# Kernel tuning notes

Measured on AMD Instinct MI355X. Metric: run time of the kernel, lower is better.

The kernel has to match this reference:

```python
import jax, jax.numpy as jnp
import numpy as np
from jax.scipy.special import logsumexp

B, S, V, T = 32, 128, 8, 66  # batch, seq_len, predicates per example, num_tags


def setup_inputs() -> dict:
    key = jax.random.key(0)
    k0, k1, k2, k3, k4, k5 = jax.random.split(key, 6)
    score = jax.random.normal(k0, (B, S, S, T), dtype=jnp.float32)
    v_label = jax.random.randint(k1, (B, V), 0, S)
    role_label = jax.random.randint(k2, (B, V, S), 0, T)
    transitions = jax.random.normal(k3, (T, T), dtype=jnp.float32) * 0.1
    start_transitions = jax.random.normal(k4, (T,), dtype=jnp.float32) * 0.1
    end_transitions = jax.random.normal(k5, (T,), dtype=jnp.float32) * 0.1
    return {
        "score": score,
        "transitions": transitions,
        "start_transitions": start_transitions,
        "end_transitions": end_transitions,
        "v_label": v_label,
        "role_label": role_label,
    }


def reference(score, transitions, start_transitions, end_transitions, v_label, role_label):
    b, s, _, t = score.shape
    v = v_label.shape[1]
    # gather predicate rows: a_score[i] = score[i].index_select(0, v_label[i])  -> [B*V, S, T]
    emissions = jnp.take_along_axis(score, v_label[:, :, None, None], axis=1).reshape(b * v, s, t)
    tags = role_label.reshape(b * v, s)

    # --- gold (numerator) score ---
    emit_sc = jnp.take_along_axis(emissions, tags[..., None], axis=-1).squeeze(-1).sum(-1)  # [BV]
    trans_sc = transitions[tags[:, :-1], tags[:, 1:]].sum(-1)  # [BV]
    gold = start_transitions[tags[:, 0]] + emit_sc + trans_sc + end_transitions[tags[:, -1]]

    # --- log partition via forward algorithm (fused logsumexp scan) ---
    alpha0 = start_transitions[None, :] + emissions[:, 0]  # [BV, T]

    def step(alpha, emit_t):
        # alpha[:, i] + transitions[i, j] -> logsumexp over i, add emission at t
        alpha = logsumexp(alpha[:, :, None] + transitions[None, :, :], axis=1) + emit_t
        return alpha, None

    alphaT, _ = jax.lax.scan(step, alpha0, jnp.swapaxes(emissions[:, 1:], 0, 1))
    log_z = logsumexp(alphaT + end_transitions[None, :], axis=-1)  # [BV]

    nll = jnp.sum(log_z - gold)
    normalizer = jnp.asarray(b * v, dtype=nll.dtype)  # num_prop with gold predicates
    return nll / normalizer
```

## Files before the change

### kernel.cpp

```cpp
#include <hip/hip_runtime.h>
#include <hip/hip_bf16.h>

constexpr int TT = 66;
constexpr int SS = 128;
constexpr int NV = 8;

__device__ __forceinline__ float rl(float v, int lane) {
    return __int_as_float(__builtin_amdgcn_readlane(__float_as_int(v), lane));
}

__global__ __launch_bounds__(128) void crf_chain_kernel(
    const float* __restrict__ score,
    const float* __restrict__ trans,
    const float* __restrict__ startt,
    const float* __restrict__ endt,
    const int*   __restrict__ v_label,
    const int*   __restrict__ role_label,
    float*       __restrict__ ws_nll)
{
    __shared__ __align__(16) float xl[SS * TT];
    __shared__ float gbuf[TT + 2];
    const int tid  = threadIdx.x;
    const int lane = tid & 63;
    const int wid  = tid >> 6;
    const int bv   = blockIdx.x;
    const int b    = bv >> 3;
    const int v    = bv & 7;

    const int prow = v_label[b * NV + v];
    const float* src = score + ((size_t)(b * SS + prow) * (SS * TT));
    const float4* src4 = reinterpret_cast<const float4*>(src);
    float4* dst4 = reinterpret_cast<float4*>(xl);
    const int base4 = wid * 1056;
    #pragma unroll
    for (int k = 0; k < 16; ++k) {
        const int idx = base4 + k * 64 + lane;
        float4 tv = src4[idx];
        tv.x = __expf(tv.x); tv.y = __expf(tv.y);
        tv.z = __expf(tv.z); tv.w = __expf(tv.w);
        dst4[idx] = tv;
    }
    if (lane < 32) {
        const int idx = base4 + 1024 + lane;
        float4 tv = src4[idx];
        tv.x = __expf(tv.x); tv.y = __expf(tv.y);
        tv.z = __expf(tv.z); tv.w = __expf(tv.w);
        dst4[idx] = tv;
    }

    const int* tags = role_label + bv * SS;
    float gold = 0.f;
    if (wid == 0) {
        const int s0 = lane;
        const int tg0 = tags[s0];
        gold += src[s0 * TT + tg0];
        gold += trans[tg0 * TT + tags[s0 + 1]];
        const int s1 = lane + 64;
        const int tg1 = tags[s1];
        gold += src[s1 * TT + tg1];
        if (lane < 63) gold += trans[tg1 * TT + tags[s1 + 1]];
        #pragma unroll
        for (int off = 32; off; off >>= 1) gold += __shfl_xor(gold, off);
        gold += startt[tags[0]] + endt[tags[SS - 1]];
    }

    const int xsel = (lane == 1) ? 65 : 64;
    float W[TT], W2[TT];
    if (wid == 0) {
        #pragma unroll
        for (int i = 0; i < TT; ++i) {
            W[i]  = __expf(trans[i * TT + lane]);
            W2[i] = __expf(trans[i * TT + xsel]);
        }
    } else {
        #pragma unroll
        for (int j = 0; j < TT; ++j) {
            W[j]  = __expf(trans[lane * TT + j]);
            W2[j] = __expf(trans[xsel * TT + j]);
        }
    }

    int esum = 0;
    float F = 0.f, F64 = 0.f, F65 = 0.f;
    if (wid == 0) {
        F   = __expf(startt[lane]) * xl[lane];
        F64 = __expf(startt[64])   * xl[64];
        F65 = __expf(startt[65])   * xl[65];
        float xc   = xl[TT + lane];
        float xc64 = xl[TT + 64];
        float xc65 = xl[TT + 65];
        #pragma unroll 1
        for (int t = 1; t <= 63; ++t) {
            const int tn = (t < 63) ? t + 1 : t;
            const float xn   = xl[tn * TT + lane];
            const float xn64 = xl[tn * TT + 64];
            const float xn65 = xl[tn * TT + 65];

            float acc0 = F64 * W[64],  acc1 = F65 * W[65];
            float acc2 = 0.f,          acc3 = 0.f;
            float ex0  = F64 * W2[64], ex1  = F65 * W2[65];
            float ex2  = 0.f,          ex3  = 0.f;
            #pragma unroll
            for (int i = 0; i < 64; i += 4) {
                const float a0 = rl(F, i + 0);
                const float a1 = rl(F, i + 1);
                const float a2 = rl(F, i + 2);
                const float a3 = rl(F, i + 3);
                acc0 = fmaf(a0, W[i + 0], acc0);  ex0 = fmaf(a0, W2[i + 0], ex0);
                acc1 = fmaf(a1, W[i + 1], acc1);  ex1 = fmaf(a1, W2[i + 1], ex1);
                acc2 = fmaf(a2, W[i + 2], acc2);  ex2 = fmaf(a2, W2[i + 2], ex2);
                acc3 = fmaf(a3, W[i + 3], acc3);  ex3 = fmaf(a3, W2[i + 3], ex3);
            }
            const float S  = (acc0 + acc1) + (acc2 + acc3);
            const float Sx = (ex0 + ex1) + (ex2 + ex3);
            const float S64 = rl(Sx, 0);
            const float S65 = rl(Sx, 1);

            const int sbits = __builtin_amdgcn_readfirstlane(__float_as_int(S));
            const int e = ((sbits >> 23) & 0xff) - 127;
            esum += e;
            const float r = __int_as_float((127 - e) << 23);

            F   = (S   * r) * xc;
            F64 = (S64 * r) * xc64;
            F65 = (S65 * r) * xc65;
            xc = xn; xc64 = xn64; xc65 = xn65;
        }
    } else {
        float G   = __expf(endt[lane]);
        float G64 = __expf(endt[64]);
        float G65 = __expf(endt[65]);
        float xc   = xl[127 * TT + lane];
        float xc64 = xl[127 * TT + 64];
        float xc65 = xl[127 * TT + 65];
        #pragma unroll 1
        for (int t = 127; t >= 64; --t) {
            const int tn = (t > 64) ? t - 1 : t;
            const float xn   = xl[tn * TT + lane];
            const float xn64 = xl[tn * TT + 64];
            const float xn65 = xl[tn * TT + 65];

            const float Y   = G * xc;
            const float Y64 = G64 * xc64;
            const float Y65 = G65 * xc65;

            float acc0 = Y64 * W[64],  acc1 = Y65 * W[65];
            float acc2 = 0.f,          acc3 = 0.f;
            float ex0  = Y64 * W2[64], ex1  = Y65 * W2[65];
            float ex2  = 0.f,          ex3  = 0.f;
            #pragma unroll
            for (int j = 0; j < 64; j += 4) {
                const float y0 = rl(Y, j + 0);
                const float y1 = rl(Y, j + 1);
                const float y2 = rl(Y, j + 2);
                const float y3 = rl(Y, j + 3);
                acc0 = fmaf(y0, W[j + 0], acc0);  ex0 = fmaf(y0, W2[j + 0], ex0);
                acc1 = fmaf(y1, W[j + 1], acc1);  ex1 = fmaf(y1, W2[j + 1], ex1);
                acc2 = fmaf(y2, W[j + 2], acc2);  ex2 = fmaf(y2, W2[j + 2], ex2);
                acc3 = fmaf(y3, W[j + 3], acc3);  ex3 = fmaf(y3, W2[j + 3], ex3);
            }
            const float S  = (acc0 + acc1) + (acc2 + acc3);
            const float Sx = (ex0 + ex1) + (ex2 + ex3);
            const float S64 = rl(Sx, 0);
            const float S65 = rl(Sx, 1);

            const int sbits = __builtin_amdgcn_readfirstlane(__float_as_int(S));
            const int e = ((sbits >> 23) & 0xff) - 127;
            esum += e;
            const float r = __int_as_float((127 - e) << 23);

            G   = S   * r;
            G64 = S64 * r;
            G65 = S65 * r;
            xc = xn; xc64 = xn64; xc65 = xn65;
        }
        gbuf[lane] = G;
        if (lane == 0) {
            gbuf[64] = G64;
            gbuf[65] = G65;
            gbuf[66] = __int_as_float(esum);
        }
    }

    __syncthreads();

    if (wid == 0) {
        float prod = F * gbuf[lane];
        #pragma unroll
        for (int off = 32; off; off >>= 1) prod += __shfl_xor(prod, off);
        const float tot = prod + F64 * gbuf[64] + F65 * gbuf[65];
        const int esumG = __float_as_int(gbuf[66]);
        const float log_z = (float)(esum + esumG) * 0.69314718056f + __logf(tot);
        if (lane == 0) ws_nll[bv] = log_z - gold;
    }
}

__global__ __launch_bounds__(64) void crf_reduce_kernel(
    const float* __restrict__ ws_nll, float* __restrict__ out)
{
    const int lane = threadIdx.x;
    float s = ws_nll[lane] + ws_nll[lane + 64] + ws_nll[lane + 128] + ws_nll[lane + 192];
    #pragma unroll
    for (int off = 32; off; off >>= 1) s += __shfl_xor(s, off);
    if (lane == 0) out[0] = s * (1.0f / 256.0f);
}

extern "C" void kernel_launch(void* const* d_in, const int* in_sizes, int n_in,
                              void* d_out, int out_size, void* d_ws, size_t ws_size,
                              hipStream_t stream) {
    const float* score  = (const float*)d_in[0];
    const float* trans  = (const float*)d_in[1];
    const float* startt = (const float*)d_in[2];
    const float* endt   = (const float*)d_in[3];
    const int*   v_label    = (const int*)d_in[4];
    const int*   role_label = (const int*)d_in[5];
    float* out = (float*)d_out;
    float* ws  = (float*)d_ws;

    crf_chain_kernel<<<256, 128, 0, stream>>>(score, trans, startt, endt,
                                              v_label, role_label, ws);
    crf_reduce_kernel<<<1, 64, 0, stream>>>(ws, out);
}
```

Measured before the change: 32.76 us.

## Compute extra-tag columns via DPP wave reductions and renormalize every other step

The 64 extra FMAs per step that computed the two tags beyond lane width (the W2 path) are replaced by a per-lane product with a transposed weight column, summed by a DPP wave reduction, plus explicit 2x2 corner terms. This halves the FMA work in the inner readlane loop but adds a serial reduction chain to each step's critical path. The exponent renormalization is also applied only on even steps, which shortens alternate iterations at some risk of float range overflow or underflow with larger inputs.

```diff
diff --git a/kernel.cpp b/kernel.cpp
--- a/kernel.cpp
+++ b/kernel.cpp
@@ -7,6 +7,20 @@
 
 __device__ __forceinline__ float rl(float v, int lane) {
     return __int_as_float(__builtin_amdgcn_readlane(__float_as_int(v), lane));
+}
+template <int CTRL>
+__device__ __forceinline__ float dpp_add(float x) {
+    int y = __builtin_amdgcn_update_dpp(0, __float_as_int(x), CTRL, 0xf, 0xf, true);
+    return x + __int_as_float(y);
+}
+__device__ __forceinline__ float wave_reduce_sum(float x) {
+    x = dpp_add<0x111>(x);
+    x = dpp_add<0x112>(x);
+    x = dpp_add<0x114>(x);
+    x = dpp_add<0x118>(x);
+    x = dpp_add<0x142>(x);
+    x = dpp_add<0x143>(x);
+    return x;
 }
 
 __global__ __launch_bounds__(128) void crf_chain_kernel(
@@ -64,21 +78,22 @@
         gold += startt[tags[0]] + endt[tags[SS - 1]];
     }
 
-    const int xsel = (lane == 1) ? 65 : 64;
-    float W[TT], W2[TT];
-    if (wid == 0) {
-        #pragma unroll
-        for (int i = 0; i < TT; ++i) {
-            W[i]  = __expf(trans[i * TT + lane]);
-            W2[i] = __expf(trans[i * TT + xsel]);
-        }
+    float W[TT], w64c, w65c;
+    if (wid == 0) {
+        #pragma unroll
+        for (int i = 0; i < TT; ++i) W[i] = __expf(trans[i * TT + lane]);
+        w64c = __expf(trans[lane * TT + 64]);
+        w65c = __expf(trans[lane * TT + 65]);
     } else {
         #pragma unroll
-        for (int j = 0; j < TT; ++j) {
-            W[j]  = __expf(trans[lane * TT + j]);
-            W2[j] = __expf(trans[xsel * TT + j]);
-        }
-    }
+        for (int j = 0; j < TT; ++j) W[j] = __expf(trans[lane * TT + j]);
+        w64c = __expf(trans[64 * TT + lane]);
+        w65c = __expf(trans[65 * TT + lane]);
+    }
+    const float c44 = __expf(trans[64 * TT + 64]);
+    const float c45 = __expf(trans[64 * TT + 65]);
+    const float c54 = __expf(trans[65 * TT + 64]);
+    const float c55 = __expf(trans[65 * TT + 65]);
 
     int esum = 0;
     float F = 0.f, F64 = 0.f, F65 = 0.f;
@@ -96,34 +111,37 @@
             const float xn64 = xl[tn * TT + 64];
             const float xn65 = xl[tn * TT + 65];
 
+            float p64 = F * w64c;
+            float p65 = F * w65c;
+            p64 = wave_reduce_sum(p64);
+            p65 = wave_reduce_sum(p65);
+
             float acc0 = F64 * W[64],  acc1 = F65 * W[65];
             float acc2 = 0.f,          acc3 = 0.f;
-            float ex0  = F64 * W2[64], ex1  = F65 * W2[65];
-            float ex2  = 0.f,          ex3  = 0.f;
             #pragma unroll
             for (int i = 0; i < 64; i += 4) {
-                const float a0 = rl(F, i + 0);
-                const float a1 = rl(F, i + 1);
-                const float a2 = rl(F, i + 2);
-                const float a3 = rl(F, i + 3);
-                acc0 = fmaf(a0, W[i + 0], acc0);  ex0 = fmaf(a0, W2[i + 0], ex0);
-                acc1 = fmaf(a1, W[i + 1], acc1);  ex1 = fmaf(a1, W2[i + 1], ex1);
-                acc2 = fmaf(a2, W[i + 2], acc2);  ex2 = fmaf(a2, W2[i + 2], ex2);
-                acc3 = fmaf(a3, W[i + 3], acc3);  ex3 = fmaf(a3, W2[i + 3], ex3);
-            }
-            const float S  = (acc0 + acc1) + (acc2 + acc3);
-            const float Sx = (ex0 + ex1) + (ex2 + ex3);
-            const float S64 = rl(Sx, 0);
-            const float S65 = rl(Sx, 1);
-
-            const int sbits = __builtin_amdgcn_readfirstlane(__float_as_int(S));
-            const int e = ((sbits >> 23) & 0xff) - 127;
-            esum += e;
-            const float r = __int_as_float((127 - e) << 23);
-
-            F   = (S   * r) * xc;
-            F64 = (S64 * r) * xc64;
-            F65 = (S65 * r) * xc65;
+                acc0 = fmaf(rl(F, i + 0), W[i + 0], acc0);
+                acc1 = fmaf(rl(F, i + 1), W[i + 1], acc1);
+                acc2 = fmaf(rl(F, i + 2), W[i + 2], acc2);
+                acc3 = fmaf(rl(F, i + 3), W[i + 3], acc3);
+            }
+            const float S   = (acc0 + acc1) + (acc2 + acc3);
+            const float S64 = rl(p64, 63) + F64 * c44 + F65 * c54;
+            const float S65 = rl(p65, 63) + F64 * c45 + F65 * c55;
+
+            if ((t & 1) == 0) {
+                const int sbits = __builtin_amdgcn_readfirstlane(__float_as_int(S));
+                const int e = ((sbits >> 23) & 0xff) - 127;
+                esum += e;
+                const float r = __int_as_float((127 - e) << 23);
+                F   = (S   * r) * xc;
+                F64 = (S64 * r) * xc64;
+                F65 = (S65 * r) * xc65;
+            } else {
+                F   = S   * xc;
+                F64 = S64 * xc64;
+                F65 = S65 * xc65;
+            }
             xc = xn; xc64 = xn64; xc65 = xn65;
         }
     } else {
@@ -144,34 +162,37 @@
             const float Y64 = G64 * xc64;
             const float Y65 = G65 * xc65;
 
+            float p64 = Y * w64c;
+            float p65 = Y * w65c;
+            p64 = wave_reduce_sum(p64);
+            p65 = wave_reduce_sum(p65);
+
             float acc0 = Y64 * W[64],  acc1 = Y65 * W[65];
             float acc2 = 0.f,          acc3 = 0.f;
-            float ex0  = Y64 * W2[64], ex1  = Y65 * W2[65];
-            float ex2  = 0.f,          ex3  = 0.f;
             #pragma unroll
             for (int j = 0; j < 64; j += 4) {
-                const float y0 = rl(Y, j + 0);
-                const float y1 = rl(Y, j + 1);
-                const float y2 = rl(Y, j + 2);
-                const float y3 = rl(Y, j + 3);
-                acc0 = fmaf(y0, W[j + 0], acc0);  ex0 = fmaf(y0, W2[j + 0], ex0);
-                acc1 = fmaf(y1, W[j + 1], acc1);  ex1 = fmaf(y1, W2[j + 1], ex1);
-                acc2 = fmaf(y2, W[j + 2], acc2);  ex2 = fmaf(y2, W2[j + 2], ex2);
-                acc3 = fmaf(y3, W[j + 3], acc3);  ex3 = fmaf(y3, W2[j + 3], ex3);
-            }
-            const float S  = (acc0 + acc1) + (acc2 + acc3);
-            const float Sx = (ex0 + ex1) + (ex2 + ex3);
-            const float S64 = rl(Sx, 0);
-            const float S65 = rl(Sx, 1);
-
-            const int sbits = __builtin_amdgcn_readfirstlane(__float_as_int(S));
-            const int e = ((sbits >> 23) & 0xff) - 127;
-            esum += e;
-            const float r = __int_as_float((127 - e) << 23);
-
-            G   = S   * r;
-            G64 = S64 * r;
-            G65 = S65 * r;
+                acc0 = fmaf(rl(Y, j + 0), W[j + 0], acc0);
+                acc1 = fmaf(rl(Y, j + 1), W[j + 1], acc1);
+                acc2 = fmaf(rl(Y, j + 2), W[j + 2], acc2);
+                acc3 = fmaf(rl(Y, j + 3), W[j + 3], acc3);
+            }
+            const float S   = (acc0 + acc1) + (acc2 + acc3);
+            const float S64 = rl(p64, 63) + Y64 * c44 + Y65 * c45;
+            const float S65 = rl(p65, 63) + Y64 * c54 + Y65 * c55;
+
+            if ((t & 1) == 0) {
+                const int sbits = __builtin_amdgcn_readfirstlane(__float_as_int(S));
+                const int e = ((sbits >> 23) & 0xff) - 127;
+                esum += e;
+                const float r = __int_as_float((127 - e) << 23);
+                G   = S   * r;
+                G64 = S64 * r;
+                G65 = S65 * r;
+            } else {
+                G   = S;
+                G64 = S64;
+                G65 = S65;
+            }
             xc = xn; xc64 = xn64; xc65 = xn65;
         }
         gbuf[lane] = G;
```

After: 30.16 us (median of 2 runs). -7.9%, faster.
